# Kernel optimization log

Measured on AMD Instinct MI355X. Metric: run time of the kernel, lower is better.

## Reference

```python
import jax, jax.numpy as jnp
import numpy as np

N = 10000        # nodes
E = 160000       # edges (avg degree 16)
IN = 8 * 144     # 1152
OUT = 2 * 144    # 288 per ChebConv
KS = [4, 5, 6, 7]


def setup_inputs() -> dict:
    key = jax.random.key(0)
    ks = jax.random.split(key, 10)
    x = jax.random.normal(ks[0], (N, IN), dtype=jnp.float32)
    edge_index = jax.random.randint(ks[1], (2, E), 0, N, dtype=jnp.int32)
    d = {"x": x, "edge_index": edge_index}
    for i, (name, K) in enumerate(zip(["3", "5", "7", "9"], KS)):
        d["W" + name] = jax.random.normal(ks[2 + i], (K, IN, OUT), dtype=jnp.float32) * 0.02
        d["b" + name] = jnp.zeros((OUT,), dtype=jnp.float32)
    return d


def _cheb_basis(x, edge_index, K):
    """Chebyshev basis T_0..T_{K-1} of L_hat = -D^{-1/2} A D^{-1/2} (lambda_max=2,
    as in PyG ChebConv default; self-loop term 2/lambda_max - 1 = 0)."""
    row, col = edge_index[0], edge_index[1]  # source, target
    n = x.shape[0]
    w = jnp.ones(row.shape, x.dtype)
    deg = jax.ops.segment_sum(w, row, num_segments=n)
    dinv = jnp.where(deg > 0, jax.lax.rsqrt(jnp.maximum(deg, 1e-12)), 0.0)
    norm = -(dinv[row] * dinv[col])  # [E]

    def prop(h):  # out[i] = sum_{j->i} norm_e * h[j]
        return jax.ops.segment_sum(h[row] * norm[:, None], col, num_segments=n)

    Tx = [x, prop(x)]
    for _ in range(K - 2):
        Tx.append(2.0 * prop(Tx[-1]) - Tx[-2])
    return jnp.stack(Tx[:K], axis=0)  # [K, N, F]


def reference(x, edge_index, W3, b3, W5, b5, W7, b7, W9, b9):
    T = _cheb_basis(x, edge_index, max(KS))  # shared basis; identical math per conv
    outs = []
    for W, b in ((W3, b3), (W5, b5), (W7, b7), (W9, b9)):
        K = W.shape[0]
        outs.append(jnp.einsum('knf,kfo->no', T[:K], W) + b)
    return jnp.concatenate(outs, axis=1)  # [N, 4*OUT]
```

## Files before the change

kernel.cpp:

```cpp
#include <hip/hip_runtime.h>

#define NN 10000
#define NE 160000
#define FIN 1152
#define FOUT 288
#define FOUT_TOTAL 1152
#define NF (NN * FOUT)
#define WSL (FIN * FOUT)
#define NSLICE 22

typedef __attribute__((ext_vector_type(8))) short short8;
typedef __attribute__((ext_vector_type(8))) unsigned short ushort8v;
typedef __attribute__((ext_vector_type(4))) float floatx4;

__device__ __forceinline__ unsigned short f2bf(float f) {
  unsigned int u = __float_as_uint(f);
  u += 0x7FFF + ((u >> 16) & 1);
  return (unsigned short)(u >> 16);
}
__device__ __forceinline__ float bf2f(unsigned short u) {
  return __uint_as_float(((unsigned int)u) << 16);
}

__device__ __forceinline__ void async_copy16(void* lds, const void* gmem) {
  __builtin_amdgcn_global_load_lds(
      (const __attribute__((address_space(1))) unsigned int*)gmem,
      (__attribute__((address_space(3))) unsigned int*)lds, 16, 0, 0);
}


__global__ void deg_kernel(const int* __restrict__ ei, int* __restrict__ deg,
                           int* __restrict__ indeg) {
  int e = blockIdx.x * 256 + threadIdx.x;
  if (e < NE) {
    atomicAdd(&deg[ei[e]], 1);
    atomicAdd(&indeg[ei[NE + e]], 1);
  }
}

__global__ void dinv_kernel(const int* __restrict__ deg, float* __restrict__ dinv) {
  int i = blockIdx.x * 256 + threadIdx.x;
  if (i < NN) {
    int d = deg[i];
    dinv[i] = d > 0 ? rsqrtf((float)d) : 0.0f;
  }
}

__global__ void scan_kernel(const int* __restrict__ indeg, int* __restrict__ rowptr,
                            int* __restrict__ cursor) {
  __shared__ int s[256];
  __shared__ int carry_s;
  if (threadIdx.x == 0) carry_s = 0;
  __syncthreads();
  for (int base = 0; base < NN; base += 256) {
    int i = base + threadIdx.x;
    int v = (i < NN) ? indeg[i] : 0;
    s[threadIdx.x] = v;
    __syncthreads();
    for (int off = 1; off < 256; off <<= 1) {
      int t = (threadIdx.x >= off) ? s[threadIdx.x - off] : 0;
      __syncthreads();
      s[threadIdx.x] += t;
      __syncthreads();
    }
    int excl = s[threadIdx.x] - v + carry_s;
    if (i < NN) { rowptr[i] = excl; cursor[i] = excl; }
    __syncthreads();
    if (threadIdx.x == 0) carry_s += s[255];
    __syncthreads();
  }
  if (threadIdx.x == 0) rowptr[NN] = carry_s;
}

__global__ void scatter_kernel(const int* __restrict__ ei, const float* __restrict__ dinv,
                               int* __restrict__ cursor, int* __restrict__ srcarr,
                               float* __restrict__ wn) {
  int e = blockIdx.x * 256 + threadIdx.x;
  if (e < NE) {
    int r = ei[e], c = ei[NE + e];
    int pos = atomicAdd(&cursor[c], 1);
    srcarr[pos] = r;
    wn[pos] = -(dinv[r] * dinv[c]);
  }
}

__global__ void wtrans_kernel(const float* __restrict__ W0, const float* __restrict__ W1,
                              const float* __restrict__ W2, const float* __restrict__ W3,
                              unsigned short* __restrict__ Wt) {
  int i = blockIdx.x * 256 + threadIdx.x;
  if (i >= NSLICE * WSL) return;
  int s = i / WSL;
  int rem = i - s * WSL;
  int o = rem / FIN;
  int f = rem - o * FIN;
  int c, k;
  if (s < 4)       { c = 0; k = s; }
  else if (s < 9)  { c = 1; k = s - 4; }
  else if (s < 15) { c = 2; k = s - 9; }
  else             { c = 3; k = s - 15; }
  const float* W = (c == 0) ? W0 : (c == 1) ? W1 : (c == 2) ? W2 : W3;
  Wt[i] = f2bf(W[(size_t)k * WSL + (size_t)f * FOUT + o]);
}

__global__ void xcast_kernel(const float* __restrict__ x, unsigned short* __restrict__ xb) {
  int i = blockIdx.x * 256 + threadIdx.x;
  if (i < NN * FIN / 4) {
    float4 v = *(const float4*)(x + (size_t)i * 4);
    ushort4 r;
    r.x = f2bf(v.x); r.y = f2bf(v.y); r.z = f2bf(v.z); r.w = f2bf(v.w);
    *(ushort4*)(xb + (size_t)i * 4) = r;
  }
}

__global__ __launch_bounds__(256) void gemm_mfma_kernel(
    const unsigned short* __restrict__ Xb, const unsigned short* __restrict__ Wt,
    unsigned short* __restrict__ Yall) {
  const int bx = blockIdx.x;
  const int slice = bx / 3;
  const int n0 = (bx - slice * 3) * 96;
  const int m0 = blockIdx.y * 128;

  __shared__ unsigned short As[128][64];
  __shared__ unsigned short Bs[96][64];

  const int tid = threadIdx.x;
  const int lane = tid & 63;
  const int wave = tid >> 6;
  const int wx = wave & 1;
  const int wy = wave >> 1;
  const int lm = lane & 15;
  const int hi = lane >> 4;

  floatx4 acc[4][3];
#pragma unroll
  for (int i = 0; i < 4; i++)
#pragma unroll
    for (int j = 0; j < 3; j++) acc[i][j] = (floatx4){0.f, 0.f, 0.f, 0.f};

  const unsigned short* Wbase = Wt + (size_t)slice * WSL;

  for (int f0 = 0; f0 < FIN; f0 += 64) {
    __syncthreads();
#pragma unroll
    for (int i = 0; i < 4; i++) {
      int idx = i * 256 + tid;
      int row = idx >> 3;
      int ck = idx & 7;
      int gr = m0 + row;
      gr = gr < NN ? gr : NN - 1;
      async_copy16((char*)&As[0][0] + idx * 16,
                   (const char*)Xb + ((size_t)gr * FIN + f0) * 2 + ((ck ^ (row & 7)) << 4));
    }
#pragma unroll
    for (int i = 0; i < 3; i++) {
      int idx = i * 256 + tid;
      int row = idx >> 3;
      int ck = idx & 7;
      async_copy16((char*)&Bs[0][0] + idx * 16,
                   (const char*)Wbase + ((size_t)(n0 + row) * FIN + f0) * 2 + ((ck ^ (row & 7)) << 4));
    }
    __syncthreads();
#pragma unroll
    for (int s = 0; s < 2; s++) {
      short8 a[4], b[3];
#pragma unroll
      for (int i = 0; i < 4; i++) {
        int ar = wy * 64 + i * 16 + lm;
        a[i] = *(const short8*)((const char*)&As[ar][0] + (((s * 4 + hi) ^ (ar & 7)) << 4));
      }
#pragma unroll
      for (int j = 0; j < 3; j++) {
        int br = wx * 48 + j * 16 + lm;
        b[j] = *(const short8*)((const char*)&Bs[br][0] + (((s * 4 + hi) ^ (br & 7)) << 4));
      }
#pragma unroll
      for (int i = 0; i < 4; i++)
#pragma unroll
        for (int j = 0; j < 3; j++)
          acc[i][j] = __builtin_amdgcn_mfma_f32_16x16x32_bf16(a[i], b[j], acc[i][j], 0, 0, 0);
    }
  }
  unsigned short* Yb = Yall + (size_t)slice * NF;
  const int cbase = n0 + wx * 48 + lm;
  const int rbase = (lane >> 4) * 4;
#pragma unroll
  for (int i = 0; i < 4; i++) {
#pragma unroll
    for (int r = 0; r < 4; r++) {
      int grow = m0 + wy * 64 + i * 16 + rbase + r;
      if (grow < NN) {
        unsigned short* op = Yb + (size_t)grow * FOUT + cbase;
#pragma unroll
        for (int j = 0; j < 3; j++) op[j * 16] = f2bf(acc[i][j][r]);
      }
    }
  }
}


struct StepA {
  const unsigned short* H[4];
  const unsigned short* Y[4];
  const unsigned short* P[4];
  unsigned short* D[4];
};

template <int NACT>
__global__ __launch_bounds__(576) void cl_step_fused(
    StepA a, const int* __restrict__ rowptr, const int* __restrict__ srcarr,
    const float* __restrict__ wn) {
  const int t = threadIdx.x;
  const int ln = t % 36;
  const int node = blockIdx.x * 16 + t / 36;
  if (node >= NN) return;
  const int off = ln * 8;
  const int rs = rowptr[node];
  const int re = rowptr[node + 1];
  float acc[NACT][8];
#pragma unroll
  for (int s = 0; s < NACT; s++)
#pragma unroll
    for (int q = 0; q < 8; q++) acc[s][q] = 0.f;

  constexpr int U = (NACT <= 2) ? 4 : 2;
  int p = rs;
  for (; p + U <= re; p += U) {
    int r[U];
    float w[U];
#pragma unroll
    for (int u = 0; u < U; u++) { r[u] = srcarr[p + u]; w[u] = wn[p + u]; }
    ushort8v h[U][NACT];
#pragma unroll
    for (int u = 0; u < U; u++)
#pragma unroll
      for (int s = 0; s < NACT; s++)
        h[u][s] = *(const ushort8v*)(a.H[s] + (size_t)r[u] * FOUT + off);
#pragma unroll
    for (int u = 0; u < U; u++)
#pragma unroll
      for (int s = 0; s < NACT; s++)
#pragma unroll
        for (int q = 0; q < 8; q++) acc[s][q] += w[u] * bf2f(h[u][s][q]);
  }
  for (; p < re; ++p) {
    int r = srcarr[p];
    float w = wn[p];
#pragma unroll
    for (int s = 0; s < NACT; s++) {
      ushort8v hh = *(const ushort8v*)(a.H[s] + (size_t)r * FOUT + off);
#pragma unroll
      for (int q = 0; q < 8; q++) acc[s][q] += w * bf2f(hh[q]);
    }
  }

  size_t o = (size_t)node * FOUT + off;
#pragma unroll
  for (int s = 0; s < NACT; s++) {
    ushort8v y = *(const ushort8v*)(a.Y[s] + o);
    ushort8v d;
    if (a.P[s]) {
      ushort8v pp = *(const ushort8v*)(a.P[s] + o);
#pragma unroll
      for (int q = 0; q < 8; q++) d[q] = f2bf(bf2f(y[q]) + 2.f * acc[s][q] - bf2f(pp[q]));
    } else {
#pragma unroll
      for (int q = 0; q < 8; q++) d[q] = f2bf(bf2f(y[q]) + 2.f * acc[s][q]);
    }
    *(ushort8v*)(a.D[s] + o) = d;
  }
}

struct FinalA {
  const unsigned short* H[4];
  const unsigned short* Y[4];
  const unsigned short* P[4];
  const float* B[4];
  int conv[4];
};

__global__ __launch_bounds__(576) void cl_final_fused(
    FinalA a, const int* __restrict__ rowptr, const int* __restrict__ srcarr,
    const float* __restrict__ wn, float* __restrict__ out) {
  const int t = threadIdx.x;
  const int ln = t % 36;
  const int node = blockIdx.x * 16 + t / 36;
  if (node >= NN) return;
  const int off = ln * 8;
  const int rs = rowptr[node];
  const int re = rowptr[node + 1];
  float acc[4][8];
#pragma unroll
  for (int s = 0; s < 4; s++)
#pragma unroll
    for (int q = 0; q < 8; q++) acc[s][q] = 0.f;

  constexpr int U = 2;
  int p = rs;
  for (; p + U <= re; p += U) {
    int r[U];
    float w[U];
#pragma unroll
    for (int u = 0; u < U; u++) { r[u] = srcarr[p + u]; w[u] = wn[p + u]; }
    ushort8v h[U][4];
#pragma unroll
    for (int u = 0; u < U; u++)
#pragma unroll
      for (int s = 0; s < 4; s++)
        h[u][s] = *(const ushort8v*)(a.H[s] + (size_t)r[u] * FOUT + off);
#pragma unroll
    for (int u = 0; u < U; u++)
#pragma unroll
      for (int s = 0; s < 4; s++)
#pragma unroll
        for (int q = 0; q < 8; q++) acc[s][q] += w[u] * bf2f(h[u][s][q]);
  }
  for (; p < re; ++p) {
    int r = srcarr[p];
    float w = wn[p];
#pragma unroll
    for (int s = 0; s < 4; s++) {
      ushort8v hh = *(const ushort8v*)(a.H[s] + (size_t)r * FOUT + off);
#pragma unroll
      for (int q = 0; q < 8; q++) acc[s][q] += w * bf2f(hh[q]);
    }
  }

  size_t o = (size_t)node * FOUT + off;
#pragma unroll
  for (int s = 0; s < 4; s++) {
    ushort8v y = *(const ushort8v*)(a.Y[s] + o);
    ushort8v pp = *(const ushort8v*)(a.P[s] + o);
    const float* bias = a.B[s] + off;
    float r8[8];
#pragma unroll
    for (int q = 0; q < 8; q++)
      r8[q] = bias[q] + bf2f(y[q]) + acc[s][q] - bf2f(pp[q]);
    float* op = out + (size_t)node * FOUT_TOTAL + a.conv[s] * FOUT + off;
    *(float4*)(op + 0) = make_float4(r8[0], r8[1], r8[2], r8[3]);
    *(float4*)(op + 4) = make_float4(r8[4], r8[5], r8[6], r8[7]);
  }
}


extern "C" void kernel_launch(void* const* d_in, const int* in_sizes, int n_in,
                              void* d_out, int out_size, void* d_ws, size_t ws_size,
                              hipStream_t stream) {
  const float* x = (const float*)d_in[0];
  const int* ei = (const int*)d_in[1];
  const float* W[4] = {(const float*)d_in[2], (const float*)d_in[4],
                       (const float*)d_in[6], (const float*)d_in[8]};
  const float* b[4] = {(const float*)d_in[3], (const float*)d_in[5],
                       (const float*)d_in[7], (const float*)d_in[9]};
  float* out = (float*)d_out;

  char* ws = (char*)d_ws;
  size_t off = 0;
  auto alloc = [&](size_t bytes) -> char* {
    char* p = ws + off;
    off += (bytes + 255) & ~(size_t)255;
    return p;
  };
  int* deg = (int*)alloc(NN * 4);
  int* indeg = (int*)alloc(NN * 4);
  int* rowptr = (int*)alloc((NN + 1) * 4);
  int* cursor = (int*)alloc(NN * 4);
  int* srcarr = (int*)alloc(NE * 4);
  float* wn = (float*)alloc(NE * 4);
  float* dinv = (float*)alloc(NN * 4);
  unsigned short* xb = (unsigned short*)alloc((size_t)NN * FIN * 2);
  unsigned short* Wt = (unsigned short*)alloc((size_t)NSLICE * WSL * 2);
  unsigned short* Yall = (unsigned short*)alloc((size_t)NSLICE * NF * 2);

  hipMemsetAsync(deg, 0, NN * 4, stream);
  hipMemsetAsync(indeg, 0, NN * 4, stream);

  deg_kernel<<<(NE + 255) / 256, 256, 0, stream>>>(ei, deg, indeg);
  dinv_kernel<<<(NN + 255) / 256, 256, 0, stream>>>(deg, dinv);
  scan_kernel<<<1, 256, 0, stream>>>(indeg, rowptr, cursor);
  scatter_kernel<<<(NE + 255) / 256, 256, 0, stream>>>(ei, dinv, cursor, srcarr, wn);
  wtrans_kernel<<<(NSLICE * WSL + 255) / 256, 256, 0, stream>>>(W[0], W[1], W[2], W[3], Wt);
  xcast_kernel<<<(NN * FIN / 4 + 255) / 256, 256, 0, stream>>>(x, xb);

  {
    dim3 grid(3 * NSLICE, (NN + 127) / 128);
    gemm_mfma_kernel<<<grid, 256, 0, stream>>>(xb, Wt, Yall);
  }

  const int nK[4] = {4, 5, 6, 7};
  const int st[4] = {0, 4, 9, 15};
  unsigned short* S[4];
  for (int c = 0; c < 4; c++) S[c] = xb + (size_t)c * NF;

  StepA sched[5];
  int nact[5] = {0, 0, 0, 0, 0};
  FinalA fa;

  for (int c = 3; c >= 0; c--) {
    int n = nK[c] - 1;
    int s0 = 6 - n;
    unsigned short* Yn = Yall + (size_t)(st[c] + n) * NF;
    unsigned short* A = S[c];
    for (int p = 1; p <= n; p++) {
      int s = s0 + p - 1;
      if (p < n) {
        unsigned short* H = (p & 1) ? Yn : A;
        unsigned short* D = (p & 1) ? A : Yn;
        int j = nact[s]++;
        sched[s].H[j] = H;
        sched[s].Y[j] = Yall + (size_t)(st[c] + n - p) * NF;
        sched[s].P[j] = (p == 1) ? nullptr : D;
        sched[s].D[j] = D;
      } else {
        int j = 3 - c;
        fa.H[j] = ((n - 1) & 1) ? A : Yn;
        fa.P[j] = ((n - 2) & 1) ? A : Yn;
        fa.Y[j] = Yall + (size_t)st[c] * NF;
        fa.B[j] = b[c];
        fa.conv[j] = c;
      }
    }
  }

  for (int s = 0; s < 5; s++)
    for (int j = nact[s]; j < 4; j++) {
      sched[s].H[j] = sched[s].H[0];
      sched[s].Y[j] = sched[s].Y[0];
      sched[s].P[j] = sched[s].P[0];
      sched[s].D[j] = sched[s].D[0];
    }

  const int grid_cl = NN / 16;
  for (int s = 0; s < 5; s++) {
    switch (nact[s]) {
      case 1: cl_step_fused<1><<<grid_cl, 576, 0, stream>>>(sched[s], rowptr, srcarr, wn); break;
      case 2: cl_step_fused<2><<<grid_cl, 576, 0, stream>>>(sched[s], rowptr, srcarr, wn); break;
      case 3: cl_step_fused<3><<<grid_cl, 576, 0, stream>>>(sched[s], rowptr, srcarr, wn); break;
      default: cl_step_fused<4><<<grid_cl, 576, 0, stream>>>(sched[s], rowptr, srcarr, wn); break;
    }
  }
  cl_final_fused<<<grid_cl, 576, 0, stream>>>(fa, rowptr, srcarr, wn, out);
}
```

Before: 728.3 us.

## Partition propagation features by XCD with persistent atomic work-claiming blocks

Splits the 288-wide feature dimension into 8 column groups, one per XCD. The step and final propagation kernels become persistent (512 blocks), and each block claims node chunks through an atomic counter, starting with the column group that matches its own XCC_ID. Because each XCD mostly gathers only its own column slice, the gathered neighbor data is meant to stay resident in that XCD's L2 instead of being fetched by all XCDs. The cost is extra atomics and __syncthreads per chunk, uneven 5/4-lane groups, and a divide/modulo by a runtime group count.

```diff
diff --git a/kernel.cpp b/kernel.cpp
--- a/kernel.cpp
+++ b/kernel.cpp
@@ -26,6 +26,12 @@
   __builtin_amdgcn_global_load_lds(
       (const __attribute__((address_space(1))) unsigned int*)gmem,
       (__attribute__((address_space(3))) unsigned int*)lds, 16, 0, 0);
+}
+
+__device__ __forceinline__ int xcd_id() {
+  int x;
+  asm volatile("s_getreg_b32 %0, hwreg(HW_REG_XCC_ID)" : "=s"(x));
+  return x & 7;
 }
 
 
@@ -203,70 +209,92 @@
   const unsigned short* Y[4];
   const unsigned short* P[4];
   unsigned short* D[4];
+  int goff[8], gcnt[8], npb[8], nchunk[8];
+  int* cur;
 };
 
 template <int NACT>
 __global__ __launch_bounds__(576) void cl_step_fused(
     StepA a, const int* __restrict__ rowptr, const int* __restrict__ srcarr,
     const float* __restrict__ wn) {
+  __shared__ int claim_s;
+  const int myx = xcd_id();
   const int t = threadIdx.x;
-  const int ln = t % 36;
-  const int node = blockIdx.x * 16 + t / 36;
-  if (node >= NN) return;
-  const int off = ln * 8;
-  const int rs = rowptr[node];
-  const int re = rowptr[node + 1];
-  float acc[NACT][8];
-#pragma unroll
-  for (int s = 0; s < NACT; s++)
-#pragma unroll
-    for (int q = 0; q < 8; q++) acc[s][q] = 0.f;
-
   constexpr int U = (NACT <= 2) ? 4 : 2;
-  int p = rs;
-  for (; p + U <= re; p += U) {
-    int r[U];
-    float w[U];
-#pragma unroll
-    for (int u = 0; u < U; u++) { r[u] = srcarr[p + u]; w[u] = wn[p + u]; }
-    ushort8v h[U][NACT];
-#pragma unroll
-    for (int u = 0; u < U; u++)
-#pragma unroll
-      for (int s = 0; s < NACT; s++)
-        h[u][s] = *(const ushort8v*)(a.H[s] + (size_t)r[u] * FOUT + off);
-#pragma unroll
-    for (int u = 0; u < U; u++)
-#pragma unroll
-      for (int s = 0; s < NACT; s++)
-#pragma unroll
-        for (int q = 0; q < 8; q++) acc[s][q] += w[u] * bf2f(h[u][s][q]);
-  }
-  for (; p < re; ++p) {
-    int r = srcarr[p];
-    float w = wn[p];
-#pragma unroll
-    for (int s = 0; s < NACT; s++) {
-      ushort8v hh = *(const ushort8v*)(a.H[s] + (size_t)r * FOUT + off);
-#pragma unroll
-      for (int q = 0; q < 8; q++) acc[s][q] += w * bf2f(hh[q]);
-    }
-  }
-
-  size_t o = (size_t)node * FOUT + off;
-#pragma unroll
-  for (int s = 0; s < NACT; s++) {
-    ushort8v y = *(const ushort8v*)(a.Y[s] + o);
-    ushort8v d;
-    if (a.P[s]) {
-      ushort8v pp = *(const ushort8v*)(a.P[s] + o);
-#pragma unroll
-      for (int q = 0; q < 8; q++) d[q] = f2bf(bf2f(y[q]) + 2.f * acc[s][q] - bf2f(pp[q]));
-    } else {
-#pragma unroll
-      for (int q = 0; q < 8; q++) d[q] = f2bf(bf2f(y[q]) + 2.f * acc[s][q]);
-    }
-    *(ushort8v*)(a.D[s] + o) = d;
+
+  for (int jj = 0; jj < 8; jj++) {
+    const int j = (myx + jj) & 7;
+    const int gcnt = a.gcnt[j];
+    const int goff = a.goff[j];
+    const int npb = a.npb[j];
+    const int nch = a.nchunk[j];
+    const int ln = t % gcnt;
+    const int nl = t / gcnt;
+    const int off = (goff + ln) * 8;
+    for (;;) {
+      if (t == 0) claim_s = atomicAdd(a.cur + j, 1);
+      __syncthreads();
+      const int c = claim_s;
+      __syncthreads();
+      if (c >= nch) break;
+      const int node = c * npb + nl;
+      if (nl < npb && node < NN) {
+        const int rs = rowptr[node];
+        const int re = rowptr[node + 1];
+        float acc[NACT][8];
+#pragma unroll
+        for (int s = 0; s < NACT; s++)
+#pragma unroll
+          for (int q = 0; q < 8; q++) acc[s][q] = 0.f;
+
+        int p = rs;
+        for (; p + U <= re; p += U) {
+          int r[U];
+          float w[U];
+#pragma unroll
+          for (int u = 0; u < U; u++) { r[u] = srcarr[p + u]; w[u] = wn[p + u]; }
+          ushort8v h[U][NACT];
+#pragma unroll
+          for (int u = 0; u < U; u++)
+#pragma unroll
+            for (int s = 0; s < NACT; s++)
+              h[u][s] = *(const ushort8v*)(a.H[s] + (size_t)r[u] * FOUT + off);
+#pragma unroll
+          for (int u = 0; u < U; u++)
+#pragma unroll
+            for (int s = 0; s < NACT; s++)
+#pragma unroll
+              for (int q = 0; q < 8; q++) acc[s][q] += w[u] * bf2f(h[u][s][q]);
+        }
+        for (; p < re; ++p) {
+          int r = srcarr[p];
+          float w = wn[p];
+#pragma unroll
+          for (int s = 0; s < NACT; s++) {
+            ushort8v hh = *(const ushort8v*)(a.H[s] + (size_t)r * FOUT + off);
+#pragma unroll
+            for (int q = 0; q < 8; q++) acc[s][q] += w * bf2f(hh[q]);
+          }
+        }
+
+        size_t o = (size_t)node * FOUT + off;
+#pragma unroll
+        for (int s = 0; s < NACT; s++) {
+          ushort8v y = *(const ushort8v*)(a.Y[s] + o);
+          ushort8v d;
+          if (a.P[s]) {
+            ushort8v pp = *(const ushort8v*)(a.P[s] + o);
+#pragma unroll
+            for (int q = 0; q < 8; q++)
+              d[q] = f2bf(bf2f(y[q]) + 2.f * acc[s][q] - bf2f(pp[q]));
+          } else {
+#pragma unroll
+            for (int q = 0; q < 8; q++) d[q] = f2bf(bf2f(y[q]) + 2.f * acc[s][q]);
+          }
+          *(ushort8v*)(a.D[s] + o) = d;
+        }
+      }
+    }
   }
 }
 
@@ -276,68 +304,89 @@
   const unsigned short* P[4];
   const float* B[4];
   int conv[4];
+  int goff[8], gcnt[8], npb[8], nchunk[8];
+  int* cur;
 };
 
 __global__ __launch_bounds__(576) void cl_final_fused(
     FinalA a, const int* __restrict__ rowptr, const int* __restrict__ srcarr,
     const float* __restrict__ wn, float* __restrict__ out) {
+  __shared__ int claim_s;
+  const int myx = xcd_id();
   const int t = threadIdx.x;
-  const int ln = t % 36;
-  const int node = blockIdx.x * 16 + t / 36;
-  if (node >= NN) return;
-  const int off = ln * 8;
-  const int rs = rowptr[node];
-  const int re = rowptr[node + 1];
-  float acc[4][8];
-#pragma unroll
-  for (int s = 0; s < 4; s++)
-#pragma unroll
-    for (int q = 0; q < 8; q++) acc[s][q] = 0.f;
-
   constexpr int U = 2;
-  int p = rs;
-  for (; p + U <= re; p += U) {
-    int r[U];
-    float w[U];
-#pragma unroll
-    for (int u = 0; u < U; u++) { r[u] = srcarr[p + u]; w[u] = wn[p + u]; }
-    ushort8v h[U][4];
-#pragma unroll
-    for (int u = 0; u < U; u++)
-#pragma unroll
-      for (int s = 0; s < 4; s++)
-        h[u][s] = *(const ushort8v*)(a.H[s] + (size_t)r[u] * FOUT + off);
-#pragma unroll
-    for (int u = 0; u < U; u++)
-#pragma unroll
-      for (int s = 0; s < 4; s++)
-#pragma unroll
-        for (int q = 0; q < 8; q++) acc[s][q] += w[u] * bf2f(h[u][s][q]);
-  }
-  for (; p < re; ++p) {
-    int r = srcarr[p];
-    float w = wn[p];
-#pragma unroll
-    for (int s = 0; s < 4; s++) {
-      ushort8v hh = *(const ushort8v*)(a.H[s] + (size_t)r * FOUT + off);
-#pragma unroll
-      for (int q = 0; q < 8; q++) acc[s][q] += w * bf2f(hh[q]);
-    }
-  }
-
-  size_t o = (size_t)node * FOUT + off;
-#pragma unroll
-  for (int s = 0; s < 4; s++) {
-    ushort8v y = *(const ushort8v*)(a.Y[s] + o);
-    ushort8v pp = *(const ushort8v*)(a.P[s] + o);
-    const float* bias = a.B[s] + off;
-    float r8[8];
-#pragma unroll
-    for (int q = 0; q < 8; q++)
-      r8[q] = bias[q] + bf2f(y[q]) + acc[s][q] - bf2f(pp[q]);
-    float* op = out + (size_t)node * FOUT_TOTAL + a.conv[s] * FOUT + off;
-    *(float4*)(op + 0) = make_float4(r8[0], r8[1], r8[2], r8[3]);
-    *(float4*)(op + 4) = make_float4(r8[4], r8[5], r8[6], r8[7]);
+
+  for (int jj = 0; jj < 8; jj++) {
+    const int j = (myx + jj) & 7;
+    const int gcnt = a.gcnt[j];
+    const int goff = a.goff[j];
+    const int npb = a.npb[j];
+    const int nch = a.nchunk[j];
+    const int ln = t % gcnt;
+    const int nl = t / gcnt;
+    const int off = (goff + ln) * 8;
+    for (;;) {
+      if (t == 0) claim_s = atomicAdd(a.cur + j, 1);
+      __syncthreads();
+      const int c = claim_s;
+      __syncthreads();
+      if (c >= nch) break;
+      const int node = c * npb + nl;
+      if (nl < npb && node < NN) {
+        const int rs = rowptr[node];
+        const int re = rowptr[node + 1];
+        float acc[4][8];
+#pragma unroll
+        for (int s = 0; s < 4; s++)
+#pragma unroll
+          for (int q = 0; q < 8; q++) acc[s][q] = 0.f;
+
+        int p = rs;
+        for (; p + U <= re; p += U) {
+          int r[U];
+          float w[U];
+#pragma unroll
+          for (int u = 0; u < U; u++) { r[u] = srcarr[p + u]; w[u] = wn[p + u]; }
+          ushort8v h[U][4];
+#pragma unroll
+          for (int u = 0; u < U; u++)
+#pragma unroll
+            for (int s = 0; s < 4; s++)
+              h[u][s] = *(const ushort8v*)(a.H[s] + (size_t)r[u] * FOUT + off);
+#pragma unroll
+          for (int u = 0; u < U; u++)
+#pragma unroll
+            for (int s = 0; s < 4; s++)
+#pragma unroll
+              for (int q = 0; q < 8; q++) acc[s][q] += w[u] * bf2f(h[u][s][q]);
+        }
+        for (; p < re; ++p) {
+          int r = srcarr[p];
+          float w = wn[p];
+#pragma unroll
+          for (int s = 0; s < 4; s++) {
+            ushort8v hh = *(const ushort8v*)(a.H[s] + (size_t)r * FOUT + off);
+#pragma unroll
+            for (int q = 0; q < 8; q++) acc[s][q] += w * bf2f(hh[q]);
+          }
+        }
+
+        size_t o = (size_t)node * FOUT + off;
+#pragma unroll
+        for (int s = 0; s < 4; s++) {
+          ushort8v y = *(const ushort8v*)(a.Y[s] + o);
+          ushort8v pp = *(const ushort8v*)(a.P[s] + o);
+          const float* bias = a.B[s] + off;
+          float r8[8];
+#pragma unroll
+          for (int q = 0; q < 8; q++)
+            r8[q] = bias[q] + bf2f(y[q]) + acc[s][q] - bf2f(pp[q]);
+          float* op = out + (size_t)node * FOUT_TOTAL + a.conv[s] * FOUT + off;
+          *(float4*)(op + 0) = make_float4(r8[0], r8[1], r8[2], r8[3]);
+          *(float4*)(op + 4) = make_float4(r8[4], r8[5], r8[6], r8[7]);
+        }
+      }
+    }
   }
 }
 
@@ -367,12 +416,14 @@
   int* srcarr = (int*)alloc(NE * 4);
   float* wn = (float*)alloc(NE * 4);
   float* dinv = (float*)alloc(NN * 4);
+  int* qcur = (int*)alloc(6 * 8 * 4);
   unsigned short* xb = (unsigned short*)alloc((size_t)NN * FIN * 2);
   unsigned short* Wt = (unsigned short*)alloc((size_t)NSLICE * WSL * 2);
   unsigned short* Yall = (unsigned short*)alloc((size_t)NSLICE * NF * 2);
 
   hipMemsetAsync(deg, 0, NN * 4, stream);
   hipMemsetAsync(indeg, 0, NN * 4, stream);
+  hipMemsetAsync(qcur, 0, 6 * 8 * 4, stream);
 
   deg_kernel<<<(NE + 255) / 256, 256, 0, stream>>>(ei, deg, indeg);
   dinv_kernel<<<(NN + 255) / 256, 256, 0, stream>>>(deg, dinv);
@@ -429,7 +480,27 @@
       sched[s].D[j] = sched[s].D[0];
     }
 
-  const int grid_cl = NN / 16;
+  const int GOFF[8] = {0, 5, 10, 15, 20, 24, 28, 32};
+  const int GCNT[8] = {5, 5, 5, 5, 4, 4, 4, 4};
+  int NPB[8], NCHUNK[8];
+  for (int j = 0; j < 8; j++) {
+    NPB[j] = 576 / GCNT[j];
+    NCHUNK[j] = (NN + NPB[j] - 1) / NPB[j];
+  }
+  for (int s = 0; s < 5; s++) {
+    for (int j = 0; j < 8; j++) {
+      sched[s].goff[j] = GOFF[j]; sched[s].gcnt[j] = GCNT[j];
+      sched[s].npb[j] = NPB[j];   sched[s].nchunk[j] = NCHUNK[j];
+    }
+    sched[s].cur = qcur + 8 * s;
+  }
+  for (int j = 0; j < 8; j++) {
+    fa.goff[j] = GOFF[j]; fa.gcnt[j] = GCNT[j];
+    fa.npb[j] = NPB[j];   fa.nchunk[j] = NCHUNK[j];
+  }
+  fa.cur = qcur + 8 * 5;
+
+  const int grid_cl = 512;
   for (int s = 0; s < 5; s++) {
     switch (nact[s]) {
       case 1: cl_step_fused<1><<<grid_cl, 576, 0, stream>>>(sched[s], rowptr, srcarr, wn); break;
```

Result: slower. 1.028 ms (+41.2%).
